# Optimization experiments

Measured on AMD Instinct MI355X. Metric: run time of the kernel, lower is better.

The kernel has to match this reference:

```python
import jax, jax.numpy as jnp
import numpy as np

N = 100000       # patches per slide (bag size)
D = 512          # size[1] for size_arg='big'
D_ATTN = 256     # size[2]
C = 4            # n_classes
N_REFS = 3
TP_RATE = 0.01
NP_RATE = 0.01
REF_RATE = 0.01
EPS = 1e-10


def setup_inputs() -> dict:
    key = jax.random.key(0)
    ks = jax.random.split(key, 8)
    w = lambda k, shape: jax.random.normal(k, shape, jnp.float32) * 0.02
    return {
        "h": jax.random.normal(ks[0], (N, D), jnp.float32),
        "label": jax.random.randint(ks[1], (2,), 0, C),
        "Wa": w(ks[2], (D, D_ATTN)), "ba": jnp.zeros((D_ATTN,), jnp.float32),
        "Wb": w(ks[3], (D, D_ATTN)), "bb": jnp.zeros((D_ATTN,), jnp.float32),
        "Wc": w(ks[4], (D_ATTN, C)), "bc": jnp.zeros((C,), jnp.float32),
        "Wcls": w(ks[5], (D, C)), "bcls": jnp.zeros((C,), jnp.float32),
        "Wr": w(ks[6], (N_REFS, D, C + 1)),
        "br": jnp.zeros((N_REFS, C + 1), jnp.float32),
    }


def _ce(logits, targets):
    # cross entropy with integer targets, reduction='none'
    logp = jax.nn.log_softmax(logits, axis=-1)
    return -jnp.take_along_axis(logp, targets[..., None], axis=-1)[..., 0]


def _find_candidate_loss(final_score, h, in_label, Wr, br):
    n = final_score.shape[0]
    k = max(1, int(n * TP_RATE))
    mn = final_score.min(axis=0)
    mx = final_score.max(axis=0)
    norm = (final_score - mn) / (mx - mn)                     # [N, C]
    vals, idx = jax.lax.top_k(norm.T, k)                      # [C, k]
    valid = (vals > 0.5) & in_label[:, None]                  # only classes in label
    logits = jnp.einsum('ckd,de->cke', h[idx], Wr) + br       # [C, k, C+1]
    tgt = jnp.broadcast_to(jnp.arange(C)[:, None], (C, k))
    ce_tp = _ce(logits, tgt)
    mean_score = final_score.mean(axis=1)
    k_np = int(n * NP_RATE)
    nvals, nidx = jax.lax.top_k(-mean_score, k_np)
    np_valid = (-nvals) < 0.5
    np_logits = h[nidx] @ Wr + br                             # [k_np, C+1]
    ce_np = -jax.nn.log_softmax(np_logits, axis=-1)[:, C]
    num = jnp.sum(ce_tp * valid) + jnp.sum(ce_np * np_valid)
    den = valid.sum() + np_valid.sum()
    return num / jnp.maximum(den, 1)


def _find_candidate_ref_loss(ref_score, h, in_label, Wr, br):
    n = ref_score.shape[0]
    k = max(1, int(n * REF_RATE))
    vals, idx = jax.lax.top_k(ref_score.T, k)                 # [C+1, k]
    include = jnp.concatenate([in_label, jnp.array([True])])  # bg class always included
    valid = (vals > 0.5) & include[:, None]
    logits = jnp.einsum('ckd,de->cke', h[idx], Wr) + br       # [C+1, k, C+1]
    tgt = jnp.broadcast_to(jnp.arange(C + 1)[:, None], (C + 1, k))
    ce = _ce(logits, tgt)
    return jnp.sum(ce * valid) / jnp.maximum(valid.sum(), 1)


def _forward(h, label, Wa, ba, Wb, bb, Wc, bc, Wcls, bcls, Wr, br):
    # gated attention (Attn_Net_Gated), eval mode (dropout off)
    a = jnp.tanh(h @ Wa + ba)
    b = jax.nn.sigmoid(h @ Wb + bb)
    det_logit = (a * b) @ Wc + bc                             # [N, C]
    cls_score = jax.nn.softmax(h @ Wcls + bcls, axis=1)
    det_score = jax.nn.softmax(det_logit, axis=0)             # softmax over instances
    final_score = cls_score * det_score
    in_label = jnp.any(jnp.arange(C)[:, None] == label[None, :], axis=1)  # [C] bool
    instance_loss = jnp.float32(0.0)
    ref_score = final_score
    for r in range(N_REFS):
        if r == 0:
            instance_loss = instance_loss + _find_candidate_loss(final_score, h, in_label, Wr[r], br[r])
        else:
            instance_loss = instance_loss + _find_candidate_ref_loss(ref_score, h, in_label, Wr[r], br[r])
        ref_score = jax.nn.softmax(h @ Wr[r] + br[r], axis=1)  # [N, C+1]
    Y_prob = jnp.clip(jnp.sum(final_score, axis=0), EPS, 1.0 - EPS)
    return final_score, Y_prob, ref_score, instance_loss


def reference(h, label, Wa, ba, Wb, bb, Wc, bc, Wcls, bcls, Wr, br):
    final_score, Y_prob, ref_score, instance_loss = _forward(
        h, label, Wa, ba, Wb, bb, Wc, bc, Wcls, bcls, Wr, br)
    Y_hat = jnp.argmax(Y_prob)[None]
    return final_score, Y_prob, Y_hat, ref_score, instance_loss
```

## Files before the change

### kernel.cpp

```cpp
#include <hip/hip_runtime.h>
#include <math.h>

#define NI    100000
#define KSEL  1000
#define NCOL2 640
#define HBINS 2048

#define OUT_FS   0
#define OUT_YP   400000
#define OUT_YH   400004
#define OUT_REF  400005
#define OUT_LOSS 900005

#define OFF_DET    0
#define OFF_CLS    400000
#define OFF_REF0   800000
#define OFF_REF1   1300000
#define OFF_MEAN   1800000
#define OFF_WPT    1900000
#define OFF_BPACK  2063840
#define OFF_SCAL   2064480
#define OFF_SELIDX 2064608
#define OFF_HIST   2079608

#define SC_SUMEXP 0
#define SC_YPROB  4
#define SC_FSMIN  8
#define SC_FSMAX  12
#define SC_THR    16
#define SC_INCL   20
#define SC_NUM    25
#define SC_CNT    28
#define SC_PREFIX 43
#define SC_RESTK  58

typedef short short8 __attribute__((ext_vector_type(8)));
typedef float f32x4 __attribute__((ext_vector_type(4)));

__device__ __forceinline__ unsigned fenc(float x) {
    unsigned u = __float_as_uint(x);
    return (u & 0x80000000u) ? ~u : (u | 0x80000000u);
}
__device__ __forceinline__ unsigned short f2bf(float f) {
    unsigned u = __float_as_uint(f);
    return (unsigned short)((u + 0x7FFFu + ((u >> 16) & 1u)) >> 16);
}

__global__ __launch_bounds__(256) void prep_kernel(
    const float* __restrict__ Wa, const float* __restrict__ Wb,
    const float* __restrict__ Wcls, const float* __restrict__ Wr,
    const float* __restrict__ ba, const float* __restrict__ bb,
    const float* __restrict__ bcls, const float* __restrict__ br,
    float* __restrict__ ws)
{
    const int tid0 = blockIdx.x * 256 + threadIdx.x;
    unsigned short* wpT = (unsigned short*)(ws + OFF_WPT);
    if (tid0 < NCOL2 * 512) {
        const int c = tid0 >> 9, k = tid0 & 511;
        float v = 0.f;
        if (c < 512)      { const int j = c >> 1; v = (c & 1) ? Wb[k*256 + j] : Wa[k*256 + j]; }
        else if (c < 516)   v = Wcls[k*4 + (c - 512)];
        else if (c < 531) { const int q = c - 516; v = Wr[((q/5)*512 + k)*5 + (q%5)]; }
        wpT[tid0] = f2bf(v);
    }
    if (tid0 < NCOL2) {
        float v = 0.f; const int c = tid0;
        if (c < 512)      v = (c & 1) ? bb[c >> 1] : ba[c >> 1];
        else if (c < 516) v = bcls[c - 512];
        else if (c < 531) v = br[c - 516];
        ws[OFF_BPACK + c] = v;
    }
    if (tid0 < 128) {
        unsigned* su = (unsigned*)(ws + OFF_SCAL);
        unsigned v = 0u;
        if (tid0 >= SC_FSMIN && tid0 < SC_FSMIN + 4)   v = 0xFFFFFFFFu;
        if (tid0 >= SC_RESTK && tid0 < SC_RESTK + 15)  v = (unsigned)KSEL;
        su[tid0] = v;
    }
    unsigned* hist = (unsigned*)(ws + OFF_HIST);
    if (tid0 < 15 * HBINS) hist[tid0] = 0u;
}

__global__ __launch_bounds__(512, 4) void gemm_mfma(
    const float* __restrict__ h, const unsigned short* __restrict__ wpT,
    const float* __restrict__ bpack, const float* __restrict__ Wc,
    const float* __restrict__ bc,
    float* __restrict__ det_logit, float* __restrict__ det_sumexp,
    float* __restrict__ cls_score, float* __restrict__ ref0,
    float* __restrict__ ref1, float* __restrict__ out_ref2)
{
    __shared__ alignas(16) unsigned char smem[73216];
    float* slog  = (float*)smem;
    float* sbias = (float*)(smem + 65536);
    float* sWc   = (float*)(smem + 68096);
    float* sdet  = (float*)(smem + 72192);

    const int tid  = threadIdx.x;
    const int lane = tid & 63;
    const int w    = tid >> 6;
    const int wm   = (w >> 2) * 32;
    const int wn   = (w & 3) * 32;
    const int lrow = lane & 15, lq = lane >> 4;
    const int row_base = blockIdx.x * 64;

    for (int t = tid; t < 640;  t += 512) sbias[t] = bpack[t];
    for (int t = tid; t < 1024; t += 512) sWc[t]   = Wc[t];
    if (tid < 64) { sdet[tid*4+0] = 0.f; sdet[tid*4+1] = 0.f; sdet[tid*4+2] = 0.f; sdet[tid*4+3] = 0.f; }

    #pragma unroll
    for (int pass = 0; pass < 2; ++pass) {
        float4 tmp[8];
        #pragma unroll
        for (int it = 0; it < 8; ++it) {
            const int q = (pass*8 + it)*512 + tid;
            const int r = q >> 7, c4 = q & 127;
            const int grow = row_base + r;
            tmp[it] = (grow < NI) ? *(const float4*)&h[(size_t)grow * 512 + c4*4]
                                  : make_float4(0.f, 0.f, 0.f, 0.f);
        }
        #pragma unroll
        for (int it = 0; it < 8; ++it) {
            const int q = (pass*8 + it)*512 + tid;
            const int r = q >> 7, c4 = q & 127;
            const int s = (c4 >> 1) ^ (r & 7);
            ushort4 pk;
            pk.x = f2bf(tmp[it].x); pk.y = f2bf(tmp[it].y);
            pk.z = f2bf(tmp[it].z); pk.w = f2bf(tmp[it].w);
            *(ushort4*)(smem + r*1024 + (s<<4) + ((c4&1)<<3)) = pk;
        }
    }
    __syncthreads();

    const int row0 = wm + lrow;
    const int r7   = row0 & 7;
    const unsigned abase = (unsigned)(row0*1024 + ((lq ^ (r7 & 3)) << 4));
    const unsigned x64   = (unsigned)((r7 & 4) << 4);

    for (int cb = 0; cb < 5; ++cb) {
        const int n0 = cb * 128;
        const unsigned short* bp0 = wpT + (size_t)(n0 + wn + lrow) * 512 + lq*8;
        const unsigned short* bp1 = bp0 + 16*512;

        f32x4 acc[2][2];
        #pragma unroll
        for (int mt = 0; mt < 2; ++mt)
            #pragma unroll
            for (int nt = 0; nt < 2; ++nt) acc[mt][nt] = (f32x4)0.f;

        uint4 bb0[3], bb1[3];
        bb0[0] = *(const uint4*)(bp0);      bb1[0] = *(const uint4*)(bp1);
        bb0[1] = *(const uint4*)(bp0+32);   bb1[1] = *(const uint4*)(bp1+32);
        bb0[2] = *(const uint4*)(bp0+64);   bb1[2] = *(const uint4*)(bp1+64);

        #pragma unroll
        for (int s = 0; s < 16; ++s) {
            const int kc = s * 32;
            const uint4 b0 = bb0[s % 3];
            const uint4 b1 = bb1[s % 3];
            if (s + 3 < 16) {
                bb0[s % 3] = *(const uint4*)(bp0 + kc + 96);
                bb1[s % 3] = *(const uint4*)(bp1 + kc + 96);
            }
            const unsigned aoff = abase + (((unsigned)(kc*2)) ^ x64);
            const short8 af0 = *(const short8*)(smem + aoff);
            const short8 af1 = *(const short8*)(smem + aoff + 16384);
            acc[0][0] = __builtin_amdgcn_mfma_f32_16x16x32_bf16(af0, *(const short8*)&b0, acc[0][0], 0, 0, 0);
            acc[0][1] = __builtin_amdgcn_mfma_f32_16x16x32_bf16(af0, *(const short8*)&b1, acc[0][1], 0, 0, 0);
            acc[1][0] = __builtin_amdgcn_mfma_f32_16x16x32_bf16(af1, *(const short8*)&b0, acc[1][0], 0, 0, 0);
            acc[1][1] = __builtin_amdgcn_mfma_f32_16x16x32_bf16(af1, *(const short8*)&b1, acc[1][1], 0, 0, 0);
        }

        if (cb < 4) {
            #pragma unroll
            for (int mt = 0; mt < 2; ++mt) {
                #pragma unroll
                for (int reg = 0; reg < 4; ++reg) {
                    float c0 = 0.f, c1 = 0.f, c2 = 0.f, c3 = 0.f;
                    #pragma unroll
                    for (int nt = 0; nt < 2; ++nt) {
                        const int cl = wn + nt*16 + lrow;
                        const float v = acc[mt][nt][reg] + sbias[n0 + cl];
                        const float p = __shfl_xor(v, 1);
                        const float ve = (lane & 1) ? p : v;
                        const float vo = (lane & 1) ? v : p;
                        const float e2 = __expf(2.f * ve);
                        const float gate = (1.f - 2.f / (e2 + 1.f)) * (1.f / (1.f + __expf(-vo)));
                        if (!(lane & 1)) {
                            const int j = (n0 + cl) >> 1;
                            c0 += gate * sWc[j*4+0]; c1 += gate * sWc[j*4+1];
                            c2 += gate * sWc[j*4+2]; c3 += gate * sWc[j*4+3];
                        }
                    }
                    #pragma unroll
                    for (int m = 1; m <= 8; m <<= 1) {
                        c0 += __shfl_xor(c0, m); c1 += __shfl_xor(c1, m);
                        c2 += __shfl_xor(c2, m); c3 += __shfl_xor(c3, m);
                    }
                    if ((lane & 15) == 0) {
                        const int rl = wm + mt*16 + lq*4 + reg;
                        atomicAdd(&sdet[rl*4+0], c0); atomicAdd(&sdet[rl*4+1], c1);
                        atomicAdd(&sdet[rl*4+2], c2); atomicAdd(&sdet[rl*4+3], c3);
                    }
                }
            }
        } else {
            __syncthreads();
            if ((w & 3) == 0) {
                #pragma unroll
                for (int mt = 0; mt < 2; ++mt)
                    #pragma unroll
                    for (int reg = 0; reg < 4; ++reg)
                        #pragma unroll
                        for (int nt = 0; nt < 2; ++nt) {
                            const int cl = nt*16 + lrow;
                            if (cl < 19) {
                                const int row = wm + mt*16 + lq*4 + reg;
                                slog[row * 20 + cl] = acc[mt][nt][reg] + sbias[512 + cl];
                            }
                        }
            }
            __syncthreads();
            if (tid < 64) {
                const int grow = row_base + tid;
                if (grow < NI) {
                    float L[19];
                    #pragma unroll
                    for (int q = 0; q < 19; ++q) L[q] = slog[tid * 20 + q];
                    {
                        float m = fmaxf(fmaxf(L[0], L[1]), fmaxf(L[2], L[3]));
                        float e0 = __expf(L[0]-m), e1 = __expf(L[1]-m), e2 = __expf(L[2]-m), e3 = __expf(L[3]-m);
                        const float inv = 1.f / (e0 + e1 + e2 + e3);
                        cls_score[(size_t)grow*4+0] = e0*inv; cls_score[(size_t)grow*4+1] = e1*inv;
                        cls_score[(size_t)grow*4+2] = e2*inv; cls_score[(size_t)grow*4+3] = e3*inv;
                    }
                    #pragma unroll
                    for (int r = 0; r < 3; ++r) {
                        float m = L[4+5*r];
                        #pragma unroll
                        for (int e = 1; e < 5; ++e) m = fmaxf(m, L[4+5*r+e]);
                        float ev[5]; float s = 0.f;
                        #pragma unroll
                        for (int e = 0; e < 5; ++e) { ev[e] = __expf(L[4+5*r+e] - m); s += ev[e]; }
                        const float inv = 1.f / s;
                        float* dst = (r == 0) ? ref0 : ((r == 1) ? ref1 : out_ref2);
                        #pragma unroll
                        for (int e = 0; e < 5; ++e) dst[(size_t)grow*5+e] = ev[e] * inv;
                    }
                }
            }
        }
    }
    __syncthreads();

    if (w == 0) {
        const int grow = row_base + tid;
        float e0 = 0.f, e1 = 0.f, e2 = 0.f, e3 = 0.f;
        const float d0 = sdet[tid*4+0] + bc[0];
        const float d1 = sdet[tid*4+1] + bc[1];
        const float d2 = sdet[tid*4+2] + bc[2];
        const float d3 = sdet[tid*4+3] + bc[3];
        if (grow < NI) {
            float4 dv = make_float4(d0, d1, d2, d3);
            *(float4*)&det_logit[(size_t)grow * 4] = dv;
            e0 = __expf(d0); e1 = __expf(d1); e2 = __expf(d2); e3 = __expf(d3);
        }
        #pragma unroll
        for (int m = 1; m < 64; m <<= 1) {
            e0 += __shfl_xor(e0, m); e1 += __shfl_xor(e1, m);
            e2 += __shfl_xor(e2, m); e3 += __shfl_xor(e3, m);
        }
        if (lane == 0) {
            atomicAdd(&det_sumexp[0], e0); atomicAdd(&det_sumexp[1], e1);
            atomicAdd(&det_sumexp[2], e2); atomicAdd(&det_sumexp[3], e3);
        }
    }
}

__global__ __launch_bounds__(256) void final_kernel(const float* __restrict__ det_logit,
        const float* __restrict__ cls_score, const float* __restrict__ det_sumexp,
        float* __restrict__ out_fs, float* __restrict__ mean_sc, float* __restrict__ yprob_sum,
        unsigned* __restrict__ fs_min_enc, unsigned* __restrict__ fs_max_enc)
{
    __shared__ float ssum[4][4], smin[4][4], smax[4][4];
    const int i = blockIdx.x * 256 + threadIdx.x;
    const bool valid = i < NI;
    float f[4]; float tot = 0.f;
    #pragma unroll
    for (int c = 0; c < 4; ++c) {
        float v = 0.f;
        if (valid) {
            const float ds = __expf(det_logit[(size_t)i*4+c]) / det_sumexp[c];
            v = cls_score[(size_t)i*4+c] * ds;
            out_fs[(size_t)i*4+c] = v;
        }
        f[c] = v; tot += v;
    }
    if (valid) mean_sc[i] = 0.25f * tot;
    float sm[4], mn[4], mx[4];
    #pragma unroll
    for (int c = 0; c < 4; ++c) {
        sm[c] = f[c];
        mn[c] = valid ? f[c] : 3.4e38f;
        mx[c] = valid ? f[c] : -3.4e38f;
    }
    #pragma unroll
    for (int c = 0; c < 4; ++c)
        #pragma unroll
        for (int m = 1; m < 64; m <<= 1) {
            sm[c] += __shfl_xor(sm[c], m, 64);
            mn[c] = fminf(mn[c], __shfl_xor(mn[c], m, 64));
            mx[c] = fmaxf(mx[c], __shfl_xor(mx[c], m, 64));
        }
    const int w = threadIdx.x >> 6;
    if ((threadIdx.x & 63) == 0) {
        #pragma unroll
        for (int c = 0; c < 4; ++c) { ssum[w][c] = sm[c]; smin[w][c] = mn[c]; smax[w][c] = mx[c]; }
    }
    __syncthreads();
    if (threadIdx.x < 4) {
        const int c = threadIdx.x;
        float S = 0.f, MN = 3.4e38f, MX = -3.4e38f;
        #pragma unroll
        for (int w2 = 0; w2 < 4; ++w2) {
            S += ssum[w2][c]; MN = fminf(MN, smin[w2][c]); MX = fmaxf(MX, smax[w2][c]);
        }
        atomicAdd(&yprob_sum[c], S);
        atomicMin(&fs_min_enc[c], fenc(MN));
        atomicMax(&fs_max_enc[c], fenc(MX));
    }
}

__global__ void scalars_kernel(const int* __restrict__ label, float* __restrict__ out,
                               float* __restrict__ ws_scal)
{
    if (blockIdx.x == 0 && threadIdx.x == 0) {
        float* sf = ws_scal; unsigned* su = (unsigned*)ws_scal; int* si = (int*)ws_scal;
        float best = -1.f; int arg = 0;
        for (int c = 0; c < 4; ++c) {
            float v = sf[SC_YPROB + c];
            v = fminf(fmaxf(v, 1e-10f), 1.f - 1e-10f);
            out[OUT_YP + c] = v;
            if (v > best) { best = v; arg = c; }
        }
        out[OUT_YH] = (float)arg;
        for (int c = 0; c < 4; ++c) {
            unsigned ue = su[SC_FSMIN + c], ux = su[SC_FSMAX + c];
            float mn = (ue & 0x80000000u) ? __uint_as_float(ue & 0x7FFFFFFFu) : __uint_as_float(~ue);
            float mx = (ux & 0x80000000u) ? __uint_as_float(ux & 0x7FFFFFFFu) : __uint_as_float(~ux);
            sf[SC_THR + c] = mn + 0.5f * (mx - mn);
        }
        const int l0 = label[0], l1 = label[1];
        for (int c = 0; c < 4; ++c) si[SC_INCL + c] = (l0 == c || l1 == c) ? 1 : 0;
        si[SC_INCL + 4] = 1;
    }
}

__device__ __forceinline__ float sel_value(int b, int i, const float* fs, const float* mean,
                                           const float* r0, const float* r1) {
    if (b < 4)  return fs[(size_t)i*4 + b];
    if (b == 4) return mean[i];
    if (b < 10) return r0[(size_t)i*5 + (b-5)];
    return r1[(size_t)i*5 + (b-10)];
}

__global__ __launch_bounds__(256) void hist_kernel(const float* __restrict__ fs,
        const float* __restrict__ mean, const float* __restrict__ r0, const float* __restrict__ r1,
        unsigned* __restrict__ hist, const float* __restrict__ ws_scal, int shift, int width)
{
    const int b = blockIdx.x;
    const unsigned* su = (const unsigned*)ws_scal;
    const int* si = (const int*)ws_scal;
    const int c = (b < 4) ? b : ((b == 4) ? -1 : ((b < 10) ? b - 5 : b - 10));
    if (c >= 0 && !si[SC_INCL + c]) return;
    __shared__ unsigned lh[HBINS];
    const int nbins = 1 << width;
    for (int t = threadIdx.x; t < nbins; t += 256) lh[t] = 0u;
    __syncthreads();
    const int pb = shift + width;
    const unsigned prefix = su[SC_PREFIX + b];
    const unsigned mask = (unsigned)(nbins - 1);
    for (int i = blockIdx.y * 256 + threadIdx.x; i < NI; i += 8 * 256) {
        const float v = sel_value(b, i, fs, mean, r0, r1);
        const unsigned u = fenc(b == 4 ? -v : v);
        if (pb >= 32 || (u >> pb) == prefix)
            atomicAdd(&lh[(u >> shift) & mask], 1u);
    }
    __syncthreads();
    for (int t = threadIdx.x; t < nbins; t += 256)
        if (lh[t]) atomicAdd(&hist[(size_t)b * HBINS + t], lh[t]);
}

__global__ __launch_bounds__(256) void scan_kernel(unsigned* __restrict__ hist,
                                                   float* __restrict__ ws_scal, int width)
{
    __shared__ unsigned csum[256];
    const int b = blockIdx.x;
    unsigned* su = (unsigned*)ws_scal;
    unsigned* hh = hist + (size_t)b * HBINS;
    const int nbins = 1 << width;
    const int chunk = (nbins + 255) >> 8;
    unsigned s = 0;
    for (int j = 0; j < chunk; ++j) {
        const int idx = threadIdx.x * chunk + j;
        if (idx < nbins) s += hh[idx];
    }
    csum[threadIdx.x] = s;
    __syncthreads();
    if (threadIdx.x == 0) {
        const unsigned K = su[SC_RESTK + b];
        unsigned running = 0; unsigned found = 0; unsigned rem = K;
        int t;
        for (t = 255; t >= 0; --t) {
            if (running + csum[t] >= K) break;
            running += csum[t];
        }
        if (t < 0) t = 0;
        for (int j = chunk - 1; j >= 0; --j) {
            const int idx = t * chunk + j;
            if (idx >= nbins) continue;
            const unsigned cc = hh[idx];
            if (running + cc >= K) { found = (unsigned)idx; rem = K - running; break; }
            running += cc;
        }
        su[SC_RESTK + b] = rem;
        su[SC_PREFIX + b] = (su[SC_PREFIX + b] << width) | found;
    }
    __syncthreads();
    for (int t2 = threadIdx.x; t2 < nbins; t2 += 256) hh[t2] = 0u;
}

__global__ __launch_bounds__(256) void collect_kernel(const float* __restrict__ fs,
        const float* __restrict__ mean, const float* __restrict__ r0, const float* __restrict__ r1,
        float* __restrict__ ws_scal, int* __restrict__ sel_idx)
{
    const int b = blockIdx.x;
    unsigned* su = (unsigned*)ws_scal; int* si = (int*)ws_scal; float* sf = ws_scal;
    const int c = (b < 4) ? b : ((b == 4) ? -1 : ((b < 10) ? b - 5 : b - 10));
    if (c >= 0 && !si[SC_INCL + c]) return;
    const unsigned kth = su[SC_PREFIX + b];
    const float extra = (b < 4) ? sf[SC_THR + b] : 0.5f;
    for (int i = blockIdx.y * 256 + threadIdx.x; i < NI; i += 8 * 256) {
        const float v = sel_value(b, i, fs, mean, r0, r1);
        const unsigned u = fenc(b == 4 ? -v : v);
        const bool cond = (b == 4) ? (v < 0.5f) : (v > extra);
        if (u >= kth && cond) {
            const int pos = atomicAdd(&si[SC_CNT + b], 1);
            if (pos < KSEL) sel_idx[b * KSEL + pos] = i;
        }
    }
}

__global__ __launch_bounds__(256) void ce_kernel(const float* __restrict__ h,
        const float* __restrict__ Wr, const float* __restrict__ br,
        const int* __restrict__ sel_idx, float* __restrict__ ws_scal)
{
    const int* si = (const int*)ws_scal;
    float* sf = ws_scal;
    const int lane = threadIdx.x & 63;
    const int wid = (blockIdx.x * blockDim.x + threadIdx.x) >> 6;
    const int nw = (gridDim.x * blockDim.x) >> 6;
    float l0a = 0.f, l1a = 0.f, l2a = 0.f;
    for (int slot = wid; slot < 15 * KSEL; slot += nw) {
        const int b = slot / KSEL;
        const int j = slot - b * KSEL;
        const int cnt = min(si[SC_CNT + b], KSEL);
        if (j >= cnt) continue;
        const int i = sel_idx[b * KSEL + j];
        const int g = (b < 5) ? 0 : ((b < 10) ? 1 : 2);
        const int tgt = (b < 4) ? b : ((b == 4) ? 4 : ((b < 10) ? (b - 5) : (b - 10)));
        const float* hr = h + (size_t)i * 512;
        const float* wr = Wr + (size_t)g * 512 * 5;
        const int d0 = lane * 8;
        const float4 va = *(const float4*)&hr[d0];
        const float4 vb = *(const float4*)&hr[d0 + 4];
        const float hv[8] = {va.x, va.y, va.z, va.w, vb.x, vb.y, vb.z, vb.w};
        float acc[5] = {0.f, 0.f, 0.f, 0.f, 0.f};
        #pragma unroll
        for (int t = 0; t < 8; ++t) {
            const float* row = wr + (size_t)(d0 + t) * 5;
            #pragma unroll
            for (int e = 0; e < 5; ++e) acc[e] += hv[t] * row[e];
        }
        #pragma unroll
        for (int e = 0; e < 5; ++e)
            #pragma unroll
            for (int m = 1; m < 64; m <<= 1) acc[e] += __shfl_xor(acc[e], m, 64);
        if (lane == 0) {
            float l[5];
            #pragma unroll
            for (int e = 0; e < 5; ++e) l[e] = acc[e] + br[g * 5 + e];
            float mx = l[0];
            #pragma unroll
            for (int e = 1; e < 5; ++e) mx = fmaxf(mx, l[e]);
            float s = 0.f;
            #pragma unroll
            for (int e = 0; e < 5; ++e) s += __expf(l[e] - mx);
            const float ce = logf(s) + mx - l[tgt];
            if (g == 0) l0a += ce; else if (g == 1) l1a += ce; else l2a += ce;
        }
    }
    if (lane == 0) {
        if (l0a != 0.f) atomicAdd(&sf[SC_NUM + 0], l0a);
        if (l1a != 0.f) atomicAdd(&sf[SC_NUM + 1], l1a);
        if (l2a != 0.f) atomicAdd(&sf[SC_NUM + 2], l2a);
    }
}

__global__ void loss_kernel(const float* __restrict__ ws_scal, float* __restrict__ out)
{
    if (blockIdx.x == 0 && threadIdx.x == 0) {
        const int* si = (const int*)ws_scal;
        float loss = 0.f;
        for (int g = 0; g < 3; ++g) {
            int den = 0;
            for (int b = g * 5; b < g * 5 + 5; ++b) den += min(si[SC_CNT + b], KSEL);
            loss += ws_scal[SC_NUM + g] / (float)(den > 1 ? den : 1);
        }
        out[OUT_LOSS] = loss;
    }
}

extern "C" void kernel_launch(void* const* d_in, const int* in_sizes, int n_in,
                              void* d_out, int out_size, void* d_ws, size_t ws_size,
                              hipStream_t stream)
{
    const float* h    = (const float*)d_in[0];
    const int*   lab  = (const int*)d_in[1];
    const float* Wa   = (const float*)d_in[2];
    const float* ba   = (const float*)d_in[3];
    const float* Wb   = (const float*)d_in[4];
    const float* bb   = (const float*)d_in[5];
    const float* Wc   = (const float*)d_in[6];
    const float* bc   = (const float*)d_in[7];
    const float* Wcls = (const float*)d_in[8];
    const float* bcls = (const float*)d_in[9];
    const float* Wr   = (const float*)d_in[10];
    const float* br   = (const float*)d_in[11];
    float* out = (float*)d_out;
    float* ws  = (float*)d_ws;

    float* det_logit = ws + OFF_DET;
    float* cls_score = ws + OFF_CLS;
    float* ref0      = ws + OFF_REF0;
    float* ref1      = ws + OFF_REF1;
    float* mean_sc   = ws + OFF_MEAN;
    unsigned short* wpT = (unsigned short*)(ws + OFF_WPT);
    float* scal = ws + OFF_SCAL;
    int*   sel_idx = (int*)(ws + OFF_SELIDX);
    unsigned* hist = (unsigned*)(ws + OFF_HIST);

    hipLaunchKernelGGL(prep_kernel, dim3(1280), dim3(256), 0, stream,
                       Wa, Wb, Wcls, Wr, ba, bb, bcls, br, ws);
    hipLaunchKernelGGL(gemm_mfma, dim3(1563), dim3(512), 0, stream,
                       h, wpT, ws + OFF_BPACK, Wc, bc,
                       det_logit, scal + SC_SUMEXP, cls_score, ref0, ref1, out + OUT_REF);
    hipLaunchKernelGGL(final_kernel, dim3(391), dim3(256), 0, stream,
                       det_logit, cls_score, scal + SC_SUMEXP,
                       out + OUT_FS, mean_sc, scal + SC_YPROB,
                       (unsigned*)(scal) + SC_FSMIN, (unsigned*)(scal) + SC_FSMAX);
    hipLaunchKernelGGL(scalars_kernel, dim3(1), dim3(64), 0, stream, lab, out, scal);
    hipLaunchKernelGGL(hist_kernel, dim3(15, 8), dim3(256), 0, stream,
                       out + OUT_FS, mean_sc, ref0, ref1, hist, scal, 21, 11);
    hipLaunchKernelGGL(scan_kernel, dim3(15), dim3(256), 0, stream, hist, scal, 11);
    hipLaunchKernelGGL(hist_kernel, dim3(15, 8), dim3(256), 0, stream,
                       out + OUT_FS, mean_sc, ref0, ref1, hist, scal, 10, 11);
    hipLaunchKernelGGL(scan_kernel, dim3(15), dim3(256), 0, stream, hist, scal, 11);
    hipLaunchKernelGGL(hist_kernel, dim3(15, 8), dim3(256), 0, stream,
                       out + OUT_FS, mean_sc, ref0, ref1, hist, scal, 0, 10);
    hipLaunchKernelGGL(scan_kernel, dim3(15), dim3(256), 0, stream, hist, scal, 10);
    hipLaunchKernelGGL(collect_kernel, dim3(15, 8), dim3(256), 0, stream,
                       out + OUT_FS, mean_sc, ref0, ref1, scal, sel_idx);
    hipLaunchKernelGGL(ce_kernel, dim3(240), dim3(256), 0, stream, h, Wr, br, sel_idx, scal);
    hipLaunchKernelGGL(loss_kernel, dim3(1), dim3(64), 0, stream, scal, out);
}
```

Measured before the change: 737.6 us.

## Fuse radix-select passes into one kernel, pre-tile weights, prefetch A/B fragments

Merges the scalars, three histogram and scan passes and the collect step into a single select_kernel with one block per selection, and folds the loss computation into ce_kernel through a last-block ticket. This cuts launch count from thirteen to five. The weight matrix is stored pre-tiled in MFMA fragment order so B loads become contiguous per lane, A/B fragments are software-pipelined one step ahead, and h is read with nontemporal loads. The trade-off is that each selection now runs in a single block of 256 threads scanning all 100k values three times, instead of being spread over eight blocks.

Measured after the change: 1.035 ms. +40.4%, slower.

```diff
diff --git a/kernel.cpp b/kernel.cpp
--- a/kernel.cpp
+++ b/kernel.cpp
@@ -33,9 +33,11 @@
 #define SC_CNT    28
 #define SC_PREFIX 43
 #define SC_RESTK  58
+#define SC_TICKET 73
 
 typedef short short8 __attribute__((ext_vector_type(8)));
 typedef float f32x4 __attribute__((ext_vector_type(4)));
+typedef unsigned int uint32x4 __attribute__((ext_vector_type(4)));
 
 __device__ __forceinline__ unsigned fenc(float x) {
     unsigned u = __float_as_uint(x);
@@ -61,7 +63,10 @@
         if (c < 512)      { const int j = c >> 1; v = (c & 1) ? Wb[k*256 + j] : Wa[k*256 + j]; }
         else if (c < 516)   v = Wcls[k*4 + (c - 512)];
         else if (c < 531) { const int q = c - 516; v = Wr[((q/5)*512 + k)*5 + (q%5)]; }
-        wpT[tid0] = f2bf(v);
+        const int cb = c >> 7, lc = c & 127;
+        const int seg = (cb*16 + (k >> 5))*8 + ((lc >> 5) << 1) + ((lc >> 4) & 1);
+        const int di  = (seg*64 + ((k >> 3) & 3)*16 + (lc & 15))*8 + (k & 7);
+        wpT[di] = f2bf(v);
     }
     if (tid0 < NCOL2) {
         float v = 0.f; const int c = tid0;
@@ -74,11 +79,8 @@
         unsigned* su = (unsigned*)(ws + OFF_SCAL);
         unsigned v = 0u;
         if (tid0 >= SC_FSMIN && tid0 < SC_FSMIN + 4)   v = 0xFFFFFFFFu;
-        if (tid0 >= SC_RESTK && tid0 < SC_RESTK + 15)  v = (unsigned)KSEL;
         su[tid0] = v;
     }
-    unsigned* hist = (unsigned*)(ws + OFF_HIST);
-    if (tid0 < 15 * HBINS) hist[tid0] = 0u;
 }
 
 __global__ __launch_bounds__(512, 4) void gemm_mfma(
@@ -109,14 +111,15 @@
 
     #pragma unroll
     for (int pass = 0; pass < 2; ++pass) {
-        float4 tmp[8];
+        f32x4 tmp[8];
         #pragma unroll
         for (int it = 0; it < 8; ++it) {
             const int q = (pass*8 + it)*512 + tid;
             const int r = q >> 7, c4 = q & 127;
             const int grow = row_base + r;
-            tmp[it] = (grow < NI) ? *(const float4*)&h[(size_t)grow * 512 + c4*4]
-                                  : make_float4(0.f, 0.f, 0.f, 0.f);
+            tmp[it] = (grow < NI)
+                ? __builtin_nontemporal_load((const f32x4*)&h[(size_t)grow * 512 + c4*4])
+                : (f32x4)0.f;
         }
         #pragma unroll
         for (int it = 0; it < 8; ++it) {
@@ -124,8 +127,8 @@
             const int r = q >> 7, c4 = q & 127;
             const int s = (c4 >> 1) ^ (r & 7);
             ushort4 pk;
-            pk.x = f2bf(tmp[it].x); pk.y = f2bf(tmp[it].y);
-            pk.z = f2bf(tmp[it].z); pk.w = f2bf(tmp[it].w);
+            pk.x = f2bf(tmp[it][0]); pk.y = f2bf(tmp[it][1]);
+            pk.z = f2bf(tmp[it][2]); pk.w = f2bf(tmp[it][3]);
             *(ushort4*)(smem + r*1024 + (s<<4) + ((c4&1)<<3)) = pk;
         }
     }
@@ -136,10 +139,11 @@
     const unsigned abase = (unsigned)(row0*1024 + ((lq ^ (r7 & 3)) << 4));
     const unsigned x64   = (unsigned)((r7 & 4) << 4);
 
+    const unsigned short* bbase = wpT + ((w & 3) << 1) * 512 + lane * 8;
+    #define BLOAD(cb_, s_, nt_) (*(const uint32x4*)(bbase + (size_t)(((cb_)*16 + (s_))*8 + (nt_)) * 512))
+
     for (int cb = 0; cb < 5; ++cb) {
         const int n0 = cb * 128;
-        const unsigned short* bp0 = wpT + (size_t)(n0 + wn + lrow) * 512 + lq*8;
-        const unsigned short* bp1 = bp0 + 16*512;
 
         f32x4 acc[2][2];
         #pragma unroll
@@ -147,27 +151,25 @@
             #pragma unroll
             for (int nt = 0; nt < 2; ++nt) acc[mt][nt] = (f32x4)0.f;
 
-        uint4 bb0[3], bb1[3];
-        bb0[0] = *(const uint4*)(bp0);      bb1[0] = *(const uint4*)(bp1);
-        bb0[1] = *(const uint4*)(bp0+32);   bb1[1] = *(const uint4*)(bp1+32);
-        bb0[2] = *(const uint4*)(bp0+64);   bb1[2] = *(const uint4*)(bp1+64);
+        uint32x4 b0c = BLOAD(cb, 0, 0), b1c = BLOAD(cb, 0, 1);
+        short8 afn0 = *(const short8*)(smem + (abase ^ x64));
+        short8 afn1 = *(const short8*)(smem + (abase ^ x64) + 16384);
 
         #pragma unroll
         for (int s = 0; s < 16; ++s) {
-            const int kc = s * 32;
-            const uint4 b0 = bb0[s % 3];
-            const uint4 b1 = bb1[s % 3];
-            if (s + 3 < 16) {
-                bb0[s % 3] = *(const uint4*)(bp0 + kc + 96);
-                bb1[s % 3] = *(const uint4*)(bp1 + kc + 96);
-            }
-            const unsigned aoff = abase + (((unsigned)(kc*2)) ^ x64);
-            const short8 af0 = *(const short8*)(smem + aoff);
-            const short8 af1 = *(const short8*)(smem + aoff + 16384);
-            acc[0][0] = __builtin_amdgcn_mfma_f32_16x16x32_bf16(af0, *(const short8*)&b0, acc[0][0], 0, 0, 0);
-            acc[0][1] = __builtin_amdgcn_mfma_f32_16x16x32_bf16(af0, *(const short8*)&b1, acc[0][1], 0, 0, 0);
-            acc[1][0] = __builtin_amdgcn_mfma_f32_16x16x32_bf16(af1, *(const short8*)&b0, acc[1][0], 0, 0, 0);
-            acc[1][1] = __builtin_amdgcn_mfma_f32_16x16x32_bf16(af1, *(const short8*)&b1, acc[1][1], 0, 0, 0);
+            uint32x4 b0n, b1n;
+            if (s + 1 < 16) { b0n = BLOAD(cb, s + 1, 0); b1n = BLOAD(cb, s + 1, 1); }
+            const short8 a0 = afn0, a1 = afn1;
+            if (s + 1 < 16) {
+                const unsigned aoff = abase + (((unsigned)((s + 1)*64)) ^ x64);
+                afn0 = *(const short8*)(smem + aoff);
+                afn1 = *(const short8*)(smem + aoff + 16384);
+            }
+            acc[0][0] = __builtin_amdgcn_mfma_f32_16x16x32_bf16(a0, *(const short8*)&b0c, acc[0][0], 0, 0, 0);
+            acc[0][1] = __builtin_amdgcn_mfma_f32_16x16x32_bf16(a0, *(const short8*)&b1c, acc[0][1], 0, 0, 0);
+            acc[1][0] = __builtin_amdgcn_mfma_f32_16x16x32_bf16(a1, *(const short8*)&b0c, acc[1][0], 0, 0, 0);
+            acc[1][1] = __builtin_amdgcn_mfma_f32_16x16x32_bf16(a1, *(const short8*)&b1c, acc[1][1], 0, 0, 0);
+            if (s + 1 < 16) { b0c = b0n; b1c = b1n; }
         }
 
         if (cb < 4) {
@@ -274,6 +276,7 @@
             atomicAdd(&det_sumexp[2], e2); atomicAdd(&det_sumexp[3], e3);
         }
     }
+    #undef BLOAD
 }
 
 __global__ __launch_bounds__(256) void final_kernel(const float* __restrict__ det_logit,
@@ -330,31 +333,6 @@
     }
 }
 
-__global__ void scalars_kernel(const int* __restrict__ label, float* __restrict__ out,
-                               float* __restrict__ ws_scal)
-{
-    if (blockIdx.x == 0 && threadIdx.x == 0) {
-        float* sf = ws_scal; unsigned* su = (unsigned*)ws_scal; int* si = (int*)ws_scal;
-        float best = -1.f; int arg = 0;
-        for (int c = 0; c < 4; ++c) {
-            float v = sf[SC_YPROB + c];
-            v = fminf(fmaxf(v, 1e-10f), 1.f - 1e-10f);
-            out[OUT_YP + c] = v;
-            if (v > best) { best = v; arg = c; }
-        }
-        out[OUT_YH] = (float)arg;
-        for (int c = 0; c < 4; ++c) {
-            unsigned ue = su[SC_FSMIN + c], ux = su[SC_FSMAX + c];
-            float mn = (ue & 0x80000000u) ? __uint_as_float(ue & 0x7FFFFFFFu) : __uint_as_float(~ue);
-            float mx = (ux & 0x80000000u) ? __uint_as_float(ux & 0x7FFFFFFFu) : __uint_as_float(~ux);
-            sf[SC_THR + c] = mn + 0.5f * (mx - mn);
-        }
-        const int l0 = label[0], l1 = label[1];
-        for (int c = 0; c < 4; ++c) si[SC_INCL + c] = (l0 == c || l1 == c) ? 1 : 0;
-        si[SC_INCL + 4] = 1;
-    }
-}
-
 __device__ __forceinline__ float sel_value(int b, int i, const float* fs, const float* mean,
                                            const float* r0, const float* r1) {
     if (b < 4)  return fs[(size_t)i*4 + b];
@@ -363,86 +341,93 @@
     return r1[(size_t)i*5 + (b-10)];
 }
 
-__global__ __launch_bounds__(256) void hist_kernel(const float* __restrict__ fs,
-        const float* __restrict__ mean, const float* __restrict__ r0, const float* __restrict__ r1,
-        unsigned* __restrict__ hist, const float* __restrict__ ws_scal, int shift, int width)
+__global__ __launch_bounds__(256) void select_kernel(
+        const float* __restrict__ fs, const float* __restrict__ mean,
+        const float* __restrict__ r0, const float* __restrict__ r1,
+        const int* __restrict__ label, float* __restrict__ out,
+        float* __restrict__ ws_scal, int* __restrict__ sel_idx)
 {
+    float* sf = ws_scal; unsigned* su = (unsigned*)ws_scal; int* si = (int*)ws_scal;
     const int b = blockIdx.x;
-    const unsigned* su = (const unsigned*)ws_scal;
-    const int* si = (const int*)ws_scal;
+    const int tid = threadIdx.x;
+
+    if (b == 0 && tid == 0) {
+        float best = -1.f; int arg = 0;
+        for (int c2 = 0; c2 < 4; ++c2) {
+            float v = sf[SC_YPROB + c2];
+            v = fminf(fmaxf(v, 1e-10f), 1.f - 1e-10f);
+            out[OUT_YP + c2] = v;
+            if (v > best) { best = v; arg = c2; }
+        }
+        out[OUT_YH] = (float)arg;
+    }
+
     const int c = (b < 4) ? b : ((b == 4) ? -1 : ((b < 10) ? b - 5 : b - 10));
-    if (c >= 0 && !si[SC_INCL + c]) return;
+    const int l0 = label[0], l1 = label[1];
+    if (c >= 0 && c != 4 && c != l0 && c != l1) return;
+
+    float thr;
+    if (b < 4) {
+        const unsigned ue = su[SC_FSMIN + b], ux = su[SC_FSMAX + b];
+        const float mn = (ue & 0x80000000u) ? __uint_as_float(ue & 0x7FFFFFFFu) : __uint_as_float(~ue);
+        const float mx = (ux & 0x80000000u) ? __uint_as_float(ux & 0x7FFFFFFFu) : __uint_as_float(~ux);
+        thr = mn + 0.5f * (mx - mn);
+    } else thr = 0.5f;
+
     __shared__ unsigned lh[HBINS];
-    const int nbins = 1 << width;
-    for (int t = threadIdx.x; t < nbins; t += 256) lh[t] = 0u;
-    __syncthreads();
-    const int pb = shift + width;
-    const unsigned prefix = su[SC_PREFIX + b];
-    const unsigned mask = (unsigned)(nbins - 1);
-    for (int i = blockIdx.y * 256 + threadIdx.x; i < NI; i += 8 * 256) {
+    __shared__ unsigned csum[256];
+    __shared__ unsigned sbc[2];
+    unsigned prefix = 0, K = KSEL;
+    const int shifts[3] = {21, 10, 0};
+    const int widths[3] = {11, 11, 10};
+    for (int p = 0; p < 3; ++p) {
+        const int shift = shifts[p], width = widths[p];
+        const int nbins = 1 << width;
+        const unsigned mask = (unsigned)(nbins - 1);
+        const int pb = shift + width;
+        for (int t = tid; t < nbins; t += 256) lh[t] = 0u;
+        __syncthreads();
+        for (int i = tid; i < NI; i += 256) {
+            const float v = sel_value(b, i, fs, mean, r0, r1);
+            const unsigned u = fenc(b == 4 ? -v : v);
+            if (pb >= 32 || (u >> pb) == prefix)
+                atomicAdd(&lh[(u >> shift) & mask], 1u);
+        }
+        __syncthreads();
+        const int chunk = (nbins + 255) >> 8;
+        unsigned s = 0;
+        for (int j = 0; j < chunk; ++j) {
+            const int idx = tid * chunk + j;
+            if (idx < nbins) s += lh[idx];
+        }
+        csum[tid] = s;
+        __syncthreads();
+        if (tid == 0) {
+            unsigned running = 0, found = 0, rem = K;
+            int t;
+            for (t = 255; t >= 0; --t) {
+                if (running + csum[t] >= K) break;
+                running += csum[t];
+            }
+            if (t < 0) t = 0;
+            for (int j = chunk - 1; j >= 0; --j) {
+                const int idx = t * chunk + j;
+                if (idx >= nbins) continue;
+                const unsigned cc2 = lh[idx];
+                if (running + cc2 >= K) { found = (unsigned)idx; rem = K - running; break; }
+                running += cc2;
+            }
+            sbc[0] = (prefix << width) | found;
+            sbc[1] = rem;
+        }
+        __syncthreads();
+        prefix = sbc[0]; K = sbc[1];
+    }
+    const unsigned kth = prefix;
+    for (int i = tid; i < NI; i += 256) {
         const float v = sel_value(b, i, fs, mean, r0, r1);
         const unsigned u = fenc(b == 4 ? -v : v);
-        if (pb >= 32 || (u >> pb) == prefix)
-            atomicAdd(&lh[(u >> shift) & mask], 1u);
-    }
-    __syncthreads();
-    for (int t = threadIdx.x; t < nbins; t += 256)
-        if (lh[t]) atomicAdd(&hist[(size_t)b * HBINS + t], lh[t]);
-}
-
-__global__ __launch_bounds__(256) void scan_kernel(unsigned* __restrict__ hist,
-                                                   float* __restrict__ ws_scal, int width)
-{
-    __shared__ unsigned csum[256];
-    const int b = blockIdx.x;
-    unsigned* su = (unsigned*)ws_scal;
-    unsigned* hh = hist + (size_t)b * HBINS;
-    const int nbins = 1 << width;
-    const int chunk = (nbins + 255) >> 8;
-    unsigned s = 0;
-    for (int j = 0; j < chunk; ++j) {
-        const int idx = threadIdx.x * chunk + j;
-        if (idx < nbins) s += hh[idx];
-    }
-    csum[threadIdx.x] = s;
-    __syncthreads();
-    if (threadIdx.x == 0) {
-        const unsigned K = su[SC_RESTK + b];
-        unsigned running = 0; unsigned found = 0; unsigned rem = K;
-        int t;
-        for (t = 255; t >= 0; --t) {
-            if (running + csum[t] >= K) break;
-            running += csum[t];
-        }
-        if (t < 0) t = 0;
-        for (int j = chunk - 1; j >= 0; --j) {
-            const int idx = t * chunk + j;
-            if (idx >= nbins) continue;
-            const unsigned cc = hh[idx];
-            if (running + cc >= K) { found = (unsigned)idx; rem = K - running; break; }
-            running += cc;
-        }
-        su[SC_RESTK + b] = rem;
-        su[SC_PREFIX + b] = (su[SC_PREFIX + b] << width) | found;
-    }
-    __syncthreads();
-    for (int t2 = threadIdx.x; t2 < nbins; t2 += 256) hh[t2] = 0u;
-}
-
-__global__ __launch_bounds__(256) void collect_kernel(const float* __restrict__ fs,
-        const float* __restrict__ mean, const float* __restrict__ r0, const float* __restrict__ r1,
-        float* __restrict__ ws_scal, int* __restrict__ sel_idx)
-{
-    const int b = blockIdx.x;
-    unsigned* su = (unsigned*)ws_scal; int* si = (int*)ws_scal; float* sf = ws_scal;
-    const int c = (b < 4) ? b : ((b == 4) ? -1 : ((b < 10) ? b - 5 : b - 10));
-    if (c >= 0 && !si[SC_INCL + c]) return;
-    const unsigned kth = su[SC_PREFIX + b];
-    const float extra = (b < 4) ? sf[SC_THR + b] : 0.5f;
-    for (int i = blockIdx.y * 256 + threadIdx.x; i < NI; i += 8 * 256) {
-        const float v = sel_value(b, i, fs, mean, r0, r1);
-        const unsigned u = fenc(b == 4 ? -v : v);
-        const bool cond = (b == 4) ? (v < 0.5f) : (v > extra);
+        const bool cond = (b == 4) ? (v < 0.5f) : (v > thr);
         if (u >= kth && cond) {
             const int pos = atomicAdd(&si[SC_CNT + b], 1);
             if (pos < KSEL) sel_idx[b * KSEL + pos] = i;
@@ -452,9 +437,10 @@
 
 __global__ __launch_bounds__(256) void ce_kernel(const float* __restrict__ h,
         const float* __restrict__ Wr, const float* __restrict__ br,
-        const int* __restrict__ sel_idx, float* __restrict__ ws_scal)
+        const int* __restrict__ sel_idx, float* __restrict__ ws_scal,
+        float* __restrict__ out)
 {
-    const int* si = (const int*)ws_scal;
+    int* si = (int*)ws_scal;
     float* sf = ws_scal;
     const int lane = threadIdx.x & 63;
     const int wid = (blockIdx.x * blockDim.x + threadIdx.x) >> 6;
@@ -504,19 +490,22 @@
         if (l1a != 0.f) atomicAdd(&sf[SC_NUM + 1], l1a);
         if (l2a != 0.f) atomicAdd(&sf[SC_NUM + 2], l2a);
     }
-}
-
-__global__ void loss_kernel(const float* __restrict__ ws_scal, float* __restrict__ out)
-{
-    if (blockIdx.x == 0 && threadIdx.x == 0) {
-        const int* si = (const int*)ws_scal;
-        float loss = 0.f;
-        for (int g = 0; g < 3; ++g) {
-            int den = 0;
-            for (int b = g * 5; b < g * 5 + 5; ++b) den += min(si[SC_CNT + b], KSEL);
-            loss += ws_scal[SC_NUM + g] / (float)(den > 1 ? den : 1);
-        }
-        out[OUT_LOSS] = loss;
+    __syncthreads();
+    if (threadIdx.x == 0) {
+        __threadfence();
+        const unsigned t = atomicAdd(&((unsigned*)ws_scal)[SC_TICKET], 1u);
+        if (t == gridDim.x - 1) {
+            __threadfence();
+            float loss = 0.f;
+            for (int g = 0; g < 3; ++g) {
+                int den = 0;
+                for (int b2 = g * 5; b2 < g * 5 + 5; ++b2)
+                    den += min(atomicAdd(&si[SC_CNT + b2], 0), KSEL);
+                const float num = atomicAdd(&sf[SC_NUM + g], 0.f);
+                loss += num / (float)(den > 1 ? den : 1);
+            }
+            out[OUT_LOSS] = loss;
+        }
     }
 }
 
@@ -547,7 +536,6 @@
     unsigned short* wpT = (unsigned short*)(ws + OFF_WPT);
     float* scal = ws + OFF_SCAL;
     int*   sel_idx = (int*)(ws + OFF_SELIDX);
-    unsigned* hist = (unsigned*)(ws + OFF_HIST);
 
     hipLaunchKernelGGL(prep_kernel, dim3(1280), dim3(256), 0, stream,
                        Wa, Wb, Wcls, Wr, ba, bb, bcls, br, ws);
@@ -558,18 +546,8 @@
                        det_logit, cls_score, scal + SC_SUMEXP,
                        out + OUT_FS, mean_sc, scal + SC_YPROB,
                        (unsigned*)(scal) + SC_FSMIN, (unsigned*)(scal) + SC_FSMAX);
-    hipLaunchKernelGGL(scalars_kernel, dim3(1), dim3(64), 0, stream, lab, out, scal);
-    hipLaunchKernelGGL(hist_kernel, dim3(15, 8), dim3(256), 0, stream,
-                       out + OUT_FS, mean_sc, ref0, ref1, hist, scal, 21, 11);
-    hipLaunchKernelGGL(scan_kernel, dim3(15), dim3(256), 0, stream, hist, scal, 11);
-    hipLaunchKernelGGL(hist_kernel, dim3(15, 8), dim3(256), 0, stream,
-                       out + OUT_FS, mean_sc, ref0, ref1, hist, scal, 10, 11);
-    hipLaunchKernelGGL(scan_kernel, dim3(15), dim3(256), 0, stream, hist, scal, 11);
-    hipLaunchKernelGGL(hist_kernel, dim3(15, 8), dim3(256), 0, stream,
-                       out + OUT_FS, mean_sc, ref0, ref1, hist, scal, 0, 10);
-    hipLaunchKernelGGL(scan_kernel, dim3(15), dim3(256), 0, stream, hist, scal, 10);
-    hipLaunchKernelGGL(collect_kernel, dim3(15, 8), dim3(256), 0, stream,
-                       out + OUT_FS, mean_sc, ref0, ref1, scal, sel_idx);
-    hipLaunchKernelGGL(ce_kernel, dim3(240), dim3(256), 0, stream, h, Wr, br, sel_idx, scal);
-    hipLaunchKernelGGL(loss_kernel, dim3(1), dim3(64), 0, stream, scal, out);
-}
+    hipLaunchKernelGGL(select_kernel, dim3(15), dim3(256), 0, stream,
+                       out + OUT_FS, mean_sc, ref0, ref1, lab, out, scal, sel_idx);
+    hipLaunchKernelGGL(ce_kernel, dim3(240), dim3(256), 0, stream,
+                       h, Wr, br, sel_idx, scal, out);
+}
```
